# Kernel optimization log

Hardware: AMD Instinct MI355X
Metric: run time of the kernel (lower is better)

## Reference

```python
import jax, jax.numpy as jnp
import numpy as np

M, K, N = 8192, 8192, 8192  # x:[M,K], weight:[N,K]
COMBINED_SCALE = 0.75  # scaling_factor(1.5) / 2 folded, as in the Triton kernel


def setup_inputs() -> dict:
    key = jax.random.key(0)
    kx, kw = jax.random.split(key)
    x = jax.random.normal(kx, (M, K), dtype=jnp.float32)
    weight = jax.random.normal(kw, (N, K), dtype=jnp.float32)
    return {"x": x, "weight": weight}


def reference(x, weight):
    # Algebraic identity: 1.5 * sum_j((x @ W^T)/2, axis=1, keepdims=True)
    #                   = 0.75 * x @ colsum(W)
    # Column-sum of weight over its N (hidden) rows -> [K]
    wcs = jnp.sum(weight, axis=0)  # fp32 accumulation
    # Per-row dot product -> [M, 1]
    y = COMBINED_SCALE * (x @ wcs)[:, None]
    return y
```

## Files before the change

### kernel.cpp

```cpp
#include <hip/hip_runtime.h>
#include <hip/hip_bf16.h>


#define M_DIM 8192
#define K_DIM 8192
#define N_DIM 8192

#define ROWCHUNKS 128
#define ROWS_PER_CHUNK (N_DIM / ROWCHUNKS)
#define K4 (K_DIM / 4)

__global__ __launch_bounds__(256) void colsum_partial(
    const float* __restrict__ w, float* __restrict__ partial) {
    const int col4 = blockIdx.x * 256 + threadIdx.x;
    const int row0 = blockIdx.y * ROWS_PER_CHUNK;
    const float4* __restrict__ p =
        (const float4*)w + (size_t)row0 * K4 + col4;

    float4 acc = make_float4(0.f, 0.f, 0.f, 0.f);
    #pragma unroll 8
    for (int r = 0; r < ROWS_PER_CHUNK; ++r) {
        float4 v = p[(size_t)r * K4];
        acc.x += v.x; acc.y += v.y; acc.z += v.z; acc.w += v.w;
    }
    ((float4*)partial)[(size_t)blockIdx.y * K4 + col4] = acc;
}

__global__ __launch_bounds__(256) void reduce_partials(
    const float* __restrict__ partial, float* __restrict__ wcs) {
    const int col4 = blockIdx.x * 256 + threadIdx.x;
    const float4* __restrict__ p4 = (const float4*)partial;

    float4 acc = make_float4(0.f, 0.f, 0.f, 0.f);
    #pragma unroll 8
    for (int c = 0; c < ROWCHUNKS; ++c) {
        float4 v = p4[(size_t)c * K4 + col4];
        acc.x += v.x; acc.y += v.y; acc.z += v.z; acc.w += v.w;
    }
    ((float4*)wcs)[col4] = acc;
}

__global__ __launch_bounds__(256) void rowdot_kernel(
    const float* __restrict__ x, const float* __restrict__ wcs,
    float* __restrict__ y) {
    const int m = blockIdx.x;
    const float4* __restrict__ x4 = (const float4*)(x + (size_t)m * K_DIM);
    const float4* __restrict__ w4 = (const float4*)wcs;

    float acc = 0.f;
    #pragma unroll 8
    for (int i = threadIdx.x; i < K4; i += 256) {
        float4 a = x4[i];
        float4 b = w4[i];
        acc += a.x * b.x + a.y * b.y + a.z * b.z + a.w * b.w;
    }
    #pragma unroll
    for (int off = 32; off > 0; off >>= 1)
        acc += __shfl_down(acc, off, 64);

    __shared__ float sacc[4];
    const int lane = threadIdx.x & 63;
    const int wave = threadIdx.x >> 6;
    if (lane == 0) sacc[wave] = acc;
    __syncthreads();
    if (threadIdx.x == 0) {
        y[m] = 0.75f * (sacc[0] + sacc[1] + sacc[2] + sacc[3]);
    }
}

extern "C" void kernel_launch(void* const* d_in, const int* in_sizes, int n_in,
                              void* d_out, int out_size, void* d_ws, size_t ws_size,
                              hipStream_t stream) {
    const float* x = (const float*)d_in[0];
    const float* w = (const float*)d_in[1];
    float* y = (float*)d_out;

    float* partial = (float*)d_ws;
    float* wcs     = (float*)d_ws + (size_t)ROWCHUNKS * K_DIM;

    dim3 g1(K4 / 256, ROWCHUNKS);
    colsum_partial<<<g1, 256, 0, stream>>>(w, partial);

    reduce_partials<<<K4 / 256, 256, 0, stream>>>(partial, wcs);

    rowdot_kernel<<<M_DIM, 256, 0, stream>>>(x, wcs, y);
}
```

Baseline: 510.0 us.

## Fuse colsum, partial reduction and row-dot into one cooperative grid-synced kernel

```diff
diff --git a/kernel.cpp b/kernel.cpp
--- a/kernel.cpp
+++ b/kernel.cpp
@@ -1,70 +1,88 @@
 #include <hip/hip_runtime.h>
+#include <hip/hip_cooperative_groups.h>
 #include <hip/hip_bf16.h>
+
+namespace cg = cooperative_groups;
 
 
 #define M_DIM 8192
 #define K_DIM 8192
 #define N_DIM 8192
+#define K4    (K_DIM / 4)
+#define NBLK  256
+#define NTHR  1024
+#define ROWCHUNKS 128
+#define RPC   (N_DIM / ROWCHUNKS)
+#define ROWS_PER_BLK (M_DIM / NBLK)
 
-#define ROWCHUNKS 128
-#define ROWS_PER_CHUNK (N_DIM / ROWCHUNKS)
-#define K4 (K_DIM / 4)
+__global__ __launch_bounds__(NTHR) void fused_kernel(
+    const float* __restrict__ x, const float* __restrict__ w,
+    float* __restrict__ partial, float* __restrict__ wcs,
+    float* __restrict__ y) {
+    cg::grid_group grid = cg::this_grid();
+    const int tid = threadIdx.x;
+    const int b = blockIdx.x;
 
-__global__ __launch_bounds__(256) void colsum_partial(
-    const float* __restrict__ w, float* __restrict__ partial) {
-    const int col4 = blockIdx.x * 256 + threadIdx.x;
-    const int row0 = blockIdx.y * ROWS_PER_CHUNK;
-    const float4* __restrict__ p =
-        (const float4*)w + (size_t)row0 * K4 + col4;
+    __shared__ float4 red[8][128];
+    __shared__ float4 swcs[K4];
 
-    float4 acc = make_float4(0.f, 0.f, 0.f, 0.f);
-    #pragma unroll 8
-    for (int r = 0; r < ROWS_PER_CHUNK; ++r) {
-        float4 v = p[(size_t)r * K4];
-        acc.x += v.x; acc.y += v.y; acc.z += v.z; acc.w += v.w;
+    {
+        const int g = b * NTHR + tid;
+        const int col4 = g & (K4 - 1);
+        const int rowchunk = g >> 11;
+        const float4* __restrict__ p =
+            (const float4*)w + (size_t)(rowchunk * RPC) * K4 + col4;
+        float4 acc = make_float4(0.f, 0.f, 0.f, 0.f);
+        #pragma unroll 8
+        for (int r = 0; r < RPC; ++r) {
+            float4 v = p[(size_t)r * K4];
+            acc.x += v.x; acc.y += v.y; acc.z += v.z; acc.w += v.w;
+        }
+        ((float4*)partial)[(size_t)rowchunk * K4 + col4] = acc;
     }
-    ((float4*)partial)[(size_t)blockIdx.y * K4 + col4] = acc;
-}
+    grid.sync();
 
-__global__ __launch_bounds__(256) void reduce_partials(
-    const float* __restrict__ partial, float* __restrict__ wcs) {
-    const int col4 = blockIdx.x * 256 + threadIdx.x;
-    const float4* __restrict__ p4 = (const float4*)partial;
+    {
+        const int j = tid >> 7;
+        const int c = tid & 127;
+        const int col4 = b * 8 + j;
+        red[j][c] = ((const float4*)partial)[(size_t)c * K4 + col4];
+        __syncthreads();
+        #pragma unroll
+        for (int s = 64; s > 0; s >>= 1) {
+            if (c < s) {
+                float4 a = red[j][c], bb = red[j][c + s];
+                a.x += bb.x; a.y += bb.y; a.z += bb.z; a.w += bb.w;
+                red[j][c] = a;
+            }
+            __syncthreads();
+        }
+        if (c == 0) ((float4*)wcs)[col4] = red[j][0];
+    }
+    grid.sync();
 
-    float4 acc = make_float4(0.f, 0.f, 0.f, 0.f);
-    #pragma unroll 8
-    for (int c = 0; c < ROWCHUNKS; ++c) {
-        float4 v = p4[(size_t)c * K4 + col4];
-        acc.x += v.x; acc.y += v.y; acc.z += v.z; acc.w += v.w;
-    }
-    ((float4*)wcs)[col4] = acc;
-}
+    {
+        for (int i = tid; i < K4; i += NTHR)
+            swcs[i] = ((const float4*)wcs)[i];
+        __syncthreads();
 
-__global__ __launch_bounds__(256) void rowdot_kernel(
-    const float* __restrict__ x, const float* __restrict__ wcs,
-    float* __restrict__ y) {
-    const int m = blockIdx.x;
-    const float4* __restrict__ x4 = (const float4*)(x + (size_t)m * K_DIM);
-    const float4* __restrict__ w4 = (const float4*)wcs;
-
-    float acc = 0.f;
-    #pragma unroll 8
-    for (int i = threadIdx.x; i < K4; i += 256) {
-        float4 a = x4[i];
-        float4 b = w4[i];
-        acc += a.x * b.x + a.y * b.y + a.z * b.z + a.w * b.w;
-    }
-    #pragma unroll
-    for (int off = 32; off > 0; off >>= 1)
-        acc += __shfl_down(acc, off, 64);
-
-    __shared__ float sacc[4];
-    const int lane = threadIdx.x & 63;
-    const int wave = threadIdx.x >> 6;
-    if (lane == 0) sacc[wave] = acc;
-    __syncthreads();
-    if (threadIdx.x == 0) {
-        y[m] = 0.75f * (sacc[0] + sacc[1] + sacc[2] + sacc[3]);
+        const int wave = tid >> 6, lane = tid & 63;
+        #pragma unroll
+        for (int rr = 0; rr < ROWS_PER_BLK / 16; ++rr) {
+            const int row = b * ROWS_PER_BLK + wave * 2 + rr;
+            const float4* __restrict__ x4 = (const float4*)x + (size_t)row * K4;
+            float acc = 0.f;
+            #pragma unroll 8
+            for (int i = lane; i < K4; i += 64) {
+                float4 a = x4[i];
+                float4 bb = swcs[i];
+                acc += a.x * bb.x + a.y * bb.y + a.z * bb.z + a.w * bb.w;
+            }
+            #pragma unroll
+            for (int off = 32; off > 0; off >>= 1)
+                acc += __shfl_down(acc, off, 64);
+            if (lane == 0) y[row] = 0.75f * acc;
+        }
     }
 }
 
@@ -78,10 +96,7 @@
     float* partial = (float*)d_ws;
     float* wcs     = (float*)d_ws + (size_t)ROWCHUNKS * K_DIM;
 
-    dim3 g1(K4 / 256, ROWCHUNKS);
-    colsum_partial<<<g1, 256, 0, stream>>>(w, partial);
-
-    reduce_partials<<<K4 / 256, 256, 0, stream>>>(partial, wcs);
-
-    rowdot_kernel<<<M_DIM, 256, 0, stream>>>(x, wcs, y);
+    void* args[] = {(void*)&x, (void*)&w, (void*)&partial, (void*)&wcs, (void*)&y};
+    hipLaunchCooperativeKernel((void*)fused_kernel, dim3(NBLK), dim3(NTHR),
+                               args, 0, stream);
 }
```

After: 570.9 us. 1.12x slower.
